# Performance work log

Hardware: AMD Instinct MI355X
Metric: run time of the kernel (lower is better)

The kernel has to match this reference:

```python
import jax, jax.numpy as jnp
import numpy as np

H = 5  # LSTM hidden size


def _lstm_layer(x, Wih, Whh, bih, bhh):
    # x: [B, T, D]; Wih: [4H, D]; Whh: [4H, H]; biases: [4H]
    B, T, _ = x.shape
    # precompute input contribution with one big GEMM (torch gate order i,f,g,o)
    xg = jnp.einsum('btd,gd->btg', x, Wih) + bih + bhh  # [B,T,4H]
    xg = jnp.swapaxes(xg, 0, 1)  # [T,B,4H]
    WhhT = Whh.T

    def step(carry, g_t):
        h, c = carry
        g = g_t + h @ WhhT
        i, f, gg, o = jnp.split(g, 4, axis=-1)
        i = jax.nn.sigmoid(i)
        f = jax.nn.sigmoid(f)
        gg = jnp.tanh(gg)
        o = jax.nn.sigmoid(o)
        c = f * c + i * gg
        h = o * jnp.tanh(c)
        return (h, c), h

    h0 = jnp.zeros((B, H), x.dtype)
    c0 = jnp.zeros((B, H), x.dtype)
    _, hs = jax.lax.scan(step, (h0, c0), xg)
    return jnp.swapaxes(hs, 0, 1)  # [B,T,H]


def _stacked_lstm(x, params):
    for (Wih, Whh, bih, bhh) in params:
        x = _lstm_layer(x, Wih, Whh, bih, bhh)
    return x


def setup_inputs() -> dict:
    key = jax.random.key(0)
    ks = jax.random.split(key, 24)
    B, T, D = 512, 1024, 225
    s = 1.0 / np.sqrt(H)

    def u(k, shape):
        return jax.random.uniform(k, shape, jnp.float32, -s, s)

    inp = {"x": jax.random.normal(ks[0], (B, T, D), jnp.float32)}
    # lstm1: layer0 input D=225, layer1 input H=5
    inp["l1_Wih0"] = u(ks[1], (4 * H, D)); inp["l1_Whh0"] = u(ks[2], (4 * H, H))
    inp["l1_bih0"] = u(ks[3], (4 * H,)); inp["l1_bhh0"] = u(ks[4], (4 * H,))
    inp["l1_Wih1"] = u(ks[5], (4 * H, H)); inp["l1_Whh1"] = u(ks[6], (4 * H, H))
    inp["l1_bih1"] = u(ks[7], (4 * H,)); inp["l1_bhh1"] = u(ks[8], (4 * H,))
    inp["fc1_W"] = u(ks[9], (H, H)); inp["fc1_b"] = u(ks[10], (H,))
    # lstm2: both layers input H=5
    inp["l2_Wih0"] = u(ks[11], (4 * H, H)); inp["l2_Whh0"] = u(ks[12], (4 * H, H))
    inp["l2_bih0"] = u(ks[13], (4 * H,)); inp["l2_bhh0"] = u(ks[14], (4 * H,))
    inp["l2_Wih1"] = u(ks[15], (4 * H, H)); inp["l2_Whh1"] = u(ks[16], (4 * H, H))
    inp["l2_bih1"] = u(ks[17], (4 * H,)); inp["l2_bhh1"] = u(ks[18], (4 * H,))
    inp["fc2_W"] = u(ks[19], (H, H)); inp["fc2_b"] = u(ks[20], (H,))
    return inp


def reference(x, l1_Wih0, l1_Whh0, l1_bih0, l1_bhh0,
              l1_Wih1, l1_Whh1, l1_bih1, l1_bhh1,
              fc1_W, fc1_b,
              l2_Wih0, l2_Whh0, l2_bih0, l2_bhh0,
              l2_Wih1, l2_Whh1, l2_bih1, l2_bhh1,
              fc2_W, fc2_b):
    # dropout layers are identity in inference mode
    h = _stacked_lstm(x, [(l1_Wih0, l1_Whh0, l1_bih0, l1_bhh0),
                          (l1_Wih1, l1_Whh1, l1_bih1, l1_bhh1)])
    h = jax.nn.relu(h @ fc1_W.T + fc1_b)
    h = _stacked_lstm(h, [(l2_Wih0, l2_Whh0, l2_bih0, l2_bhh0),
                          (l2_Wih1, l2_Whh1, l2_bih1, l2_bhh1)])
    return jax.nn.sigmoid(h @ fc2_W.T + fc2_b)
```

## Files before the change

### kernel.cpp

```cpp
#include <hip/hip_runtime.h>
#include <math.h>

#define T_STEPS 1024
#define B_SIZE  512
#define D_IN    225
#define WT_K    228
#define LOG2E   1.4426950408889634f

typedef float f32x2 __attribute__((ext_vector_type(2)));

__device__ __forceinline__ float fexp2(float x) {
#if __has_builtin(__builtin_amdgcn_exp2f)
  return __builtin_amdgcn_exp2f(x);
#else
  return exp2f(x);
#endif
}
__device__ __forceinline__ float frcp(float x) {
#if __has_builtin(__builtin_amdgcn_rcpf)
  return __builtin_amdgcn_rcpf(x);
#else
  return 1.0f / x;
#endif
}
#define SIG(x) frcp(1.0f + fexp2((x) * (-LOG2E)))
#define TH(x)  fmaf(2.0f, frcp(1.0f + fexp2((x) * (-2.0f * LOG2E))), -1.0f)

#define GL16(gp, lp) __builtin_amdgcn_global_load_lds(                          \
    (const __attribute__((address_space(1))) void*)(gp),                        \
    (__attribute__((address_space(3))) void*)(lp), 16, 0, 0)
#define GL4(gp, lp)  __builtin_amdgcn_global_load_lds(                          \
    (const __attribute__((address_space(1))) void*)(gp),                        \
    (__attribute__((address_space(3))) void*)(lp), 4, 0, 0)

#define WAIT_VM0() do {                                                         \
    asm volatile("s_waitcnt vmcnt(0)" ::: "memory");                            \
    __builtin_amdgcn_sched_barrier(0);                                          \
  } while (0)
#define WAIT_VM10() do {                                                        \
    asm volatile("s_waitcnt vmcnt(10)" ::: "memory");                           \
    __builtin_amdgcn_sched_barrier(0);                                          \
  } while (0)

__global__ __launch_bounds__(256)
void prep_wt(const float* __restrict__ Wih, const float* __restrict__ bih,
             const float* __restrict__ bhh, float* __restrict__ wt2)
{
  int i = blockIdx.x * 256 + threadIdx.x;
  int g = i / WT_K, kk = i - g * WT_K;
  float v = 0.f;
  if (g < 20 && kk < 225) v = Wih[g * 225 + kk];
  if (i >= 4560 && i < 4580) v = bih[i - 4560] + bhh[i - 4560];
  wt2[i] = v;
}

__global__ __launch_bounds__(256)
void xg_gemm(const float* __restrict__ x, const float* __restrict__ wtg,
             float* __restrict__ xg)
{
  __shared__ __align__(16) float xs[64 * 228];
  __shared__ __align__(16) float wt[4608];
  __shared__ float xs224[64];
  const int tid  = threadIdx.x;
  const int lane = tid & 63;
  const int w    = __builtin_amdgcn_readfirstlane(tid >> 6);

  for (int m = w; m < 18; m += 4)
    GL16(wtg + m * 256 + lane * 4, wt + m * 256);

  {
    const uint32_t base = (uint32_t)blockIdx.x * 57600u;
    const uint32_t lim  = 471859184u;
    for (int m = w; m < 57; m += 4) {
      uint32_t c   = (uint32_t)(m * 64 + lane);
      uint32_t r   = __umulhi(c, 75350304u);
      uint32_t off = (c << 4) - 12u * r;
      uint32_t ga  = base + off;
      ga = (ga < lim) ? ga : lim;
      GL16((const char*)x + ga, (char*)xs + m * 1024);
    }
    if (w == 0)
      GL4(x + (size_t)blockIdx.x * 14400 + lane * 225 + 224, xs224 + lane);
  }
  __syncthreads();

  const float* wr = wt + (5 * w) * WT_K;
  float acc[5];
#pragma unroll
  for (int j = 0; j < 5; ++j) acc[j] = wt[4560 + 5 * w + j];
  const float* xr = xs + lane * 228;

#pragma unroll 8
  for (int kb = 0; kb < 224; kb += 4) {
    const float4 xv = *(const float4*)(xr + kb);
#pragma unroll
    for (int j = 0; j < 5; ++j) {
      const float4 wv = *(const float4*)(wr + j * WT_K + kb);
      acc[j] = fmaf(xv.x, wv.x, acc[j]);
      acc[j] = fmaf(xv.y, wv.y, acc[j]);
      acc[j] = fmaf(xv.z, wv.z, acc[j]);
      acc[j] = fmaf(xv.w, wv.w, acc[j]);
    }
  }
  {
    float xl = xs224[lane];
#pragma unroll
    for (int j = 0; j < 5; ++j) acc[j] = fmaf(xl, wr[j * WT_K + 224], acc[j]);
  }
  float* op = xg + ((size_t)blockIdx.x * 64 + lane) * 20 + w;
#pragma unroll
  for (int j = 0; j < 5; ++j) op[4 * j] = acc[j];
}

__global__ __launch_bounds__(64)
void lstm_fused(const float* __restrict__ xg, float* __restrict__ out,
              const float* __restrict__ l1_Whh0,
              const float* __restrict__ l1_Wih1, const float* __restrict__ l1_Whh1,
              const float* __restrict__ l1_bih1, const float* __restrict__ l1_bhh1,
              const float* __restrict__ fc1_W,  const float* __restrict__ fc1_b,
              const float* __restrict__ l2_Wih0, const float* __restrict__ l2_Whh0,
              const float* __restrict__ l2_bih0, const float* __restrict__ l2_bhh0,
              const float* __restrict__ l2_Wih1, const float* __restrict__ l2_Whh1,
              const float* __restrict__ l2_bih1, const float* __restrict__ l2_bhh1,
              const float* __restrict__ fc2_W,  const float* __restrict__ fc2_b)
{
  __shared__ __align__(16) float xq[2][2][1280];
  __shared__ float outb[2][64][5];
  const int lane  = threadIdx.x & 63;
  const int half  = lane >> 5;
  const int l32   = lane & 31;
  const int stage = (l32 < 30) ? (l32 / 5) : 6;
  const int u     = (l32 < 30) ? (l32 - stage * 5) : 0;
  const int b0    = blockIdx.x * 2;

  const bool is_l0   = (stage == 0);
  const bool is_relu = (stage == 2);
  const bool is_fc   = (stage == 2) || (stage == 5);
  const bool is_fc2  = (stage == 5);

  float wi[4][5] = {}, wh[4][5] = {}, bs[4] = {};
  if (stage == 0) {
#pragma unroll
    for (int q = 0; q < 4; ++q)
#pragma unroll
      for (int j = 0; j < 5; ++j) wh[q][j] = l1_Whh0[(u + 5 * q) * 5 + j];
  } else if (stage == 1) {
#pragma unroll
    for (int q = 0; q < 4; ++q) {
#pragma unroll
      for (int j = 0; j < 5; ++j) {
        wi[q][j] = l1_Wih1[(u + 5 * q) * 5 + j];
        wh[q][j] = l1_Whh1[(u + 5 * q) * 5 + j];
      }
      bs[q] = l1_bih1[u + 5 * q] + l1_bhh1[u + 5 * q];
    }
  } else if (stage == 3) {
#pragma unroll
    for (int q = 0; q < 4; ++q) {
#pragma unroll
      for (int j = 0; j < 5; ++j) {
        wi[q][j] = l2_Wih0[(u + 5 * q) * 5 + j];
        wh[q][j] = l2_Whh0[(u + 5 * q) * 5 + j];
      }
      bs[q] = l2_bih0[u + 5 * q] + l2_bhh0[u + 5 * q];
    }
  } else if (stage == 4) {
#pragma unroll
    for (int q = 0; q < 4; ++q) {
#pragma unroll
      for (int j = 0; j < 5; ++j) {
        wi[q][j] = l2_Wih1[(u + 5 * q) * 5 + j];
        wh[q][j] = l2_Whh1[(u + 5 * q) * 5 + j];
      }
      bs[q] = l2_bih1[u + 5 * q] + l2_bhh1[u + 5 * q];
    }
  } else if (stage == 2) {
#pragma unroll
    for (int j = 0; j < 5; ++j) wi[0][j] = fc1_W[u * 5 + j];
    bs[0] = fc1_b[u];
  } else if (stage == 5) {
#pragma unroll
    for (int j = 0; j < 5; ++j) wi[0][j] = fc2_W[u * 5 + j];
    bs[0] = fc2_b[u];
  }

  f32x2 wi01[5], wi23[5], wh01[5], wh23[5];
#pragma unroll
  for (int j = 0; j < 5; ++j) {
    wi01[j] = f32x2{wi[0][j], wi[1][j]};
    wi23[j] = f32x2{wi[2][j], wi[3][j]};
    wh01[j] = f32x2{wh[0][j], wh[1][j]};
    wh23[j] = f32x2{wh[2][j], wh[3][j]};
  }
  const f32x2 bs01 = f32x2{bs[0], bs[1]};
  const f32x2 bs23 = f32x2{bs[2], bs[3]};

  int ii[5], ih[5];
  const int bse = half * 32;
  const int inb = (stage >= 1 && stage <= 5) ? (stage - 1) * 5 : 0;
  const int hb_ = (stage <= 5) ? stage * 5 : 0;
#pragma unroll
  for (int j = 0; j < 5; ++j) {
    ii[j] = (bse + inb + j) * 4;
    ih[j] = (bse + hb_ + j) * 4;
  }

  const float* obf = &outb[0][0][0];
  float* outbase = out + (size_t)b0 * T_STEPS * 5;
  int lof[10], ofs[10];
  bool fg1[10], fg2[10];
#pragma unroll
  for (int i2 = 0; i2 < 10; ++i2) {
    int idx = i2 * 64 + lane;
    int e  = (idx >= 320) ? 1 : 0;
    int r  = idx - e * 320;
    int tq = r / 5;
    int j2 = r - tq * 5;
    lof[i2] = e * 320 + (((tq - 5) & 63) * 5) + j2;
    ofs[i2] = e * (T_STEPS * 5) + tq * 5 + j2;
    fg1[i2] = (tq >= 5);
    fg2[i2] = (tq < 5);
  }

  const float* src0 = xg + (size_t)(b0 + 0) * T_STEPS * 20;
  const float* src1 = xg + (size_t)(b0 + 1) * T_STEPS * 20;

#define STAGE_CHUNK(CH, BUF)                                                   \
  { const float* s0_ = src0 + (CH) * 1280;                                     \
    const float* s1_ = src1 + (CH) * 1280;                                     \
    float* d0_ = &xq[BUF][0][0];                                               \
    float* d1_ = &xq[BUF][1][0];                                               \
    _Pragma("unroll")                                                          \
    for (int m = 0; m < 5; ++m) {                                              \
      GL16(s0_ + m * 256 + lane * 4, d0_ + m * 256);                           \
      GL16(s1_ + m * 256 + lane * 4, d1_ + m * 256);                           \
    } }

#define TICK(QV, GUARDED, KVAL)                                                \
  { const int hvi_ = __float_as_int(hv);                                       \
    float inx[5], hhx[5];                                                      \
    _Pragma("unroll")                                                          \
    for (int j = 0; j < 5; ++j) {                                              \
      inx[j] = __int_as_float(__builtin_amdgcn_ds_bpermute(ii[j], hvi_));      \
      hhx[j] = __int_as_float(__builtin_amdgcn_ds_bpermute(ih[j], hvi_));      \
    }                                                                          \
    f32x2 a01 = is_l0 ? f32x2{(QV).x, (QV).y} : bs01;                          \
    f32x2 a23 = is_l0 ? f32x2{(QV).z, (QV).w} : bs23;                          \
    f32x2 b01, b23;                                                            \
    { const f32x2 h0 = f32x2{hhx[0], hhx[0]};                                  \
      b01 = wh01[0] * h0; b23 = wh23[0] * h0; }                                \
    _Pragma("unroll")                                                          \
    for (int j = 0; j < 5; ++j) {                                              \
      const f32x2 xj = f32x2{inx[j], inx[j]};                                  \
      a01 = __builtin_elementwise_fma(wi01[j], xj, a01);                       \
      a23 = __builtin_elementwise_fma(wi23[j], xj, a23);                       \
    }                                                                          \
    _Pragma("unroll")                                                          \
    for (int j = 1; j < 5; ++j) {                                              \
      const f32x2 hj = f32x2{hhx[j], hhx[j]};                                  \
      b01 = __builtin_elementwise_fma(wh01[j], hj, b01);                       \
      b23 = __builtin_elementwise_fma(wh23[j], hj, b23);                       \
    }                                                                          \
    const f32x2 pre01 = a01 + b01, pre23 = a23 + b23;                          \
    float i_ = SIG(pre01.x), f_ = SIG(pre01.y);                                \
    float g_ = TH(pre23.x),  o_ = SIG(pre23.y);                                \
    float cn = fmaf(f_, c, i_ * g_);                                           \
    float hl = o_ * TH(cn);                                                    \
    float fx = is_relu ? fmaxf(pre01.x, 0.0f) : i_;                            \
    float hn = is_fc ? fx : hl;                                                \
    if (GUARDED) { bool ok = (KVAL) >= stage; c = ok ? cn : c; hv = ok ? hn : hv; } \
    else         { c = cn; hv = hn; }                                          \
    if (is_fc2) outb[half][((KVAL) + 59) & 63][u] = i_;                        \
  }

#define LQ(T) (*(const float4*)(xqb + 20 * (T)))
#define MINQ(X) (((X) > 63) ? 63 : (X))

#define CHUNK_BODY(GUARDED)                                                    \
  { float4 qA = LQ(0), qB = LQ(1), qC = LQ(2), qD = LQ(3);                     \
    _Pragma("unroll")                                                          \
    for (int g4 = 0; g4 < 16; ++g4) {                                          \
      const int kk = g4 * 4;                                                   \
      TICK(qA, GUARDED, kk + 0)                                                \
      qA = LQ(MINQ(kk + 4));                                                   \
      TICK(qB, GUARDED, kk + 1)                                                \
      qB = LQ(MINQ(kk + 5));                                                   \
      TICK(qC, GUARDED, kk + 2)                                                \
      qC = LQ(MINQ(kk + 6));                                                   \
      TICK(qD, GUARDED, kk + 3)                                                \
      qD = LQ(MINQ(kk + 7));                                                   \
    } }

#define FLUSH(TBASE, MODE)                                                     \
  { _Pragma("unroll")                                                          \
    for (int i2 = 0; i2 < 10; ++i2) {                                          \
      float v = obf[lof[i2]];                                                  \
      bool ok = (MODE == 0) || ((MODE == 1) ? fg1[i2] : fg2[i2]);              \
      if (ok) outbase[ofs[i2] + (TBASE) * 5] = v;                              \
    } }

  float hv = 0.f, c = 0.f;

  STAGE_CHUNK(0, 0)
  WAIT_VM0();

  {
    STAGE_CHUNK(1, 1)
    const float* xqb = &xq[0][half][4 * u];
    CHUNK_BODY(true)
    FLUSH(-5, 1)
    WAIT_VM10();
  }
  for (int ch = 1; ch < 16; ++ch) {
    if (ch < 15) STAGE_CHUNK(ch + 1, (ch + 1) & 1)
    const float* xqb = &xq[ch & 1][half][4 * u];
    CHUNK_BODY(false)
    FLUSH(ch * 64 - 5, 0)
    WAIT_VM10();
  }
  {
    const float* xqb = &xq[0][half][4 * u];
    float4 qZ = LQ(0);
    TICK(qZ, false, 0)
    TICK(qZ, false, 1)
    TICK(qZ, false, 2)
    TICK(qZ, false, 3)
    TICK(qZ, false, 4)
    FLUSH(T_STEPS - 5, 2)
  }

#undef STAGE_CHUNK
#undef TICK
#undef LQ
#undef MINQ
#undef CHUNK_BODY
#undef FLUSH
}

extern "C" void kernel_launch(void* const* d_in, const int* in_sizes, int n_in,
                              void* d_out, int out_size, void* d_ws, size_t ws_size,
                              hipStream_t stream)
{
  const float* x        = (const float*)d_in[0];
  const float* l1_Wih0  = (const float*)d_in[1];
  const float* l1_Whh0  = (const float*)d_in[2];
  const float* l1_bih0  = (const float*)d_in[3];
  const float* l1_bhh0  = (const float*)d_in[4];
  const float* l1_Wih1  = (const float*)d_in[5];
  const float* l1_Whh1  = (const float*)d_in[6];
  const float* l1_bih1  = (const float*)d_in[7];
  const float* l1_bhh1  = (const float*)d_in[8];
  const float* fc1_W    = (const float*)d_in[9];
  const float* fc1_b    = (const float*)d_in[10];
  const float* l2_Wih0  = (const float*)d_in[11];
  const float* l2_Whh0  = (const float*)d_in[12];
  const float* l2_bih0  = (const float*)d_in[13];
  const float* l2_bhh0  = (const float*)d_in[14];
  const float* l2_Wih1  = (const float*)d_in[15];
  const float* l2_Whh1  = (const float*)d_in[16];
  const float* l2_bih1  = (const float*)d_in[17];
  const float* l2_bhh1  = (const float*)d_in[18];
  const float* fc2_W    = (const float*)d_in[19];
  const float* fc2_b    = (const float*)d_in[20];

  float* xg   = (float*)d_ws;
  float* wtws = xg + 10485760;
  float* out  = (float*)d_out;

  prep_wt<<<dim3(18), dim3(256), 0, stream>>>(l1_Wih0, l1_bih0, l1_bhh0, wtws);

  xg_gemm<<<dim3((B_SIZE * T_STEPS) / 64), dim3(256), 0, stream>>>(x, wtws, xg);

  lstm_fused<<<dim3(B_SIZE / 2), dim3(64), 0, stream>>>(
      xg, out, l1_Whh0, l1_Wih1, l1_Whh1, l1_bih1, l1_bhh1,
      fc1_W, fc1_b, l2_Wih0, l2_Whh0, l2_bih0, l2_bhh0,
      l2_Wih1, l2_Whh1, l2_bih1, l2_bhh1, fc2_W, fc2_b);
}
```

Measured before the change: 414.9 us.

## Interleave two independent batch recurrences per wavefront and halve the grid

After: 649.2 us. 56.5% more time.

```diff
diff --git a/kernel.cpp b/kernel.cpp
--- a/kernel.cpp
+++ b/kernel.cpp
@@ -37,8 +37,8 @@
     asm volatile("s_waitcnt vmcnt(0)" ::: "memory");                            \
     __builtin_amdgcn_sched_barrier(0);                                          \
   } while (0)
-#define WAIT_VM10() do {                                                        \
-    asm volatile("s_waitcnt vmcnt(10)" ::: "memory");                           \
+#define WAIT_VM20() do {                                                        \
+    asm volatile("s_waitcnt vmcnt(20)" ::: "memory");                           \
     __builtin_amdgcn_sched_barrier(0);                                          \
   } while (0)
 
@@ -124,14 +124,14 @@
               const float* __restrict__ l2_bih1, const float* __restrict__ l2_bhh1,
               const float* __restrict__ fc2_W,  const float* __restrict__ fc2_b)
 {
-  __shared__ __align__(16) float xq[2][2][1280];
-  __shared__ float outb[2][64][5];
+  __shared__ __align__(16) float xq[2][4][1280];
+  __shared__ float outb[4][64][5];
   const int lane  = threadIdx.x & 63;
   const int half  = lane >> 5;
   const int l32   = lane & 31;
   const int stage = (l32 < 30) ? (l32 / 5) : 6;
   const int u     = (l32 < 30) ? (l32 - stage * 5) : 0;
-  const int b0    = blockIdx.x * 2;
+  const int b0    = blockIdx.x * 4;
 
   const bool is_l0   = (stage == 0);
   const bool is_relu = (stage == 2);
@@ -207,133 +207,131 @@
 
   const float* obf = &outb[0][0][0];
   float* outbase = out + (size_t)b0 * T_STEPS * 5;
-  int lof[10], ofs[10];
-  bool fg1[10], fg2[10];
-#pragma unroll
-  for (int i2 = 0; i2 < 10; ++i2) {
+  int lof[20], ofsv[20];
+  bool fgA[20], fgB[20];
+#pragma unroll
+  for (int i2 = 0; i2 < 20; ++i2) {
     int idx = i2 * 64 + lane;
-    int e  = (idx >= 320) ? 1 : 0;
-    int r  = idx - e * 320;
+    int m  = idx / 320;
+    int r  = idx - m * 320;
     int tq = r / 5;
     int j2 = r - tq * 5;
-    lof[i2] = e * 320 + (((tq - 5) & 63) * 5) + j2;
-    ofs[i2] = e * (T_STEPS * 5) + tq * 5 + j2;
-    fg1[i2] = (tq >= 5);
-    fg2[i2] = (tq < 5);
-  }
-
-  const float* src0 = xg + (size_t)(b0 + 0) * T_STEPS * 20;
-  const float* src1 = xg + (size_t)(b0 + 1) * T_STEPS * 20;
+    lof[i2]  = m * 320 + (((tq - 5) & 63) * 5) + j2;
+    ofsv[i2] = m * (T_STEPS * 5) + tq * 5 + j2;
+    fgA[i2]  = (tq >= 5);
+    fgB[i2]  = (tq < 5);
+  }
+
+  const float* srcp0 = xg + (size_t)(b0 + 0) * T_STEPS * 20;
+  const float* srcp1 = xg + (size_t)(b0 + 1) * T_STEPS * 20;
+  const float* srcp2 = xg + (size_t)(b0 + 2) * T_STEPS * 20;
+  const float* srcp3 = xg + (size_t)(b0 + 3) * T_STEPS * 20;
 
 #define STAGE_CHUNK(CH, BUF)                                                   \
-  { const float* s0_ = src0 + (CH) * 1280;                                     \
-    const float* s1_ = src1 + (CH) * 1280;                                     \
-    float* d0_ = &xq[BUF][0][0];                                               \
-    float* d1_ = &xq[BUF][1][0];                                               \
-    _Pragma("unroll")                                                          \
+  { _Pragma("unroll")                                                          \
     for (int m = 0; m < 5; ++m) {                                              \
-      GL16(s0_ + m * 256 + lane * 4, d0_ + m * 256);                           \
-      GL16(s1_ + m * 256 + lane * 4, d1_ + m * 256);                           \
+      GL16(srcp0 + (CH) * 1280 + m * 256 + lane * 4, &xq[BUF][0][m * 256]);    \
+      GL16(srcp1 + (CH) * 1280 + m * 256 + lane * 4, &xq[BUF][1][m * 256]);    \
+      GL16(srcp2 + (CH) * 1280 + m * 256 + lane * 4, &xq[BUF][2][m * 256]);    \
+      GL16(srcp3 + (CH) * 1280 + m * 256 + lane * 4, &xq[BUF][3][m * 256]);    \
     } }
 
-#define TICK(QV, GUARDED, KVAL)                                                \
-  { const int hvi_ = __float_as_int(hv);                                       \
-    float inx[5], hhx[5];                                                      \
+#define TICKP(Q, IN, HH, HV, CC, OB, XQB, GUARDED, KVAL)                       \
+  { f32x2 a01 = is_l0 ? f32x2{(Q).x, (Q).y} : bs01;                            \
+    f32x2 a23 = is_l0 ? f32x2{(Q).z, (Q).w} : bs23;                            \
     _Pragma("unroll")                                                          \
     for (int j = 0; j < 5; ++j) {                                              \
-      inx[j] = __int_as_float(__builtin_amdgcn_ds_bpermute(ii[j], hvi_));      \
-      hhx[j] = __int_as_float(__builtin_amdgcn_ds_bpermute(ih[j], hvi_));      \
-    }                                                                          \
-    f32x2 a01 = is_l0 ? f32x2{(QV).x, (QV).y} : bs01;                          \
-    f32x2 a23 = is_l0 ? f32x2{(QV).z, (QV).w} : bs23;                          \
-    f32x2 b01, b23;                                                            \
-    { const f32x2 h0 = f32x2{hhx[0], hhx[0]};                                  \
-      b01 = wh01[0] * h0; b23 = wh23[0] * h0; }                                \
-    _Pragma("unroll")                                                          \
-    for (int j = 0; j < 5; ++j) {                                              \
-      const f32x2 xj = f32x2{inx[j], inx[j]};                                  \
+      const f32x2 xj = f32x2{IN[j], IN[j]};                                    \
       a01 = __builtin_elementwise_fma(wi01[j], xj, a01);                       \
       a23 = __builtin_elementwise_fma(wi23[j], xj, a23);                       \
     }                                                                          \
+    f32x2 b01, b23;                                                            \
+    { const f32x2 h0 = f32x2{HH[0], HH[0]};                                    \
+      b01 = wh01[0] * h0; b23 = wh23[0] * h0; }                                \
     _Pragma("unroll")                                                          \
     for (int j = 1; j < 5; ++j) {                                              \
-      const f32x2 hj = f32x2{hhx[j], hhx[j]};                                  \
+      const f32x2 hj = f32x2{HH[j], HH[j]};                                    \
       b01 = __builtin_elementwise_fma(wh01[j], hj, b01);                       \
       b23 = __builtin_elementwise_fma(wh23[j], hj, b23);                       \
     }                                                                          \
     const f32x2 pre01 = a01 + b01, pre23 = a23 + b23;                          \
     float i_ = SIG(pre01.x), f_ = SIG(pre01.y);                                \
     float g_ = TH(pre23.x),  o_ = SIG(pre23.y);                                \
-    float cn = fmaf(f_, c, i_ * g_);                                           \
+    float cn = fmaf(f_, CC, i_ * g_);                                          \
     float hl = o_ * TH(cn);                                                    \
     float fx = is_relu ? fmaxf(pre01.x, 0.0f) : i_;                            \
     float hn = is_fc ? fx : hl;                                                \
-    if (GUARDED) { bool ok = (KVAL) >= stage; c = ok ? cn : c; hv = ok ? hn : hv; } \
-    else         { c = cn; hv = hn; }                                          \
-    if (is_fc2) outb[half][((KVAL) + 59) & 63][u] = i_;                        \
-  }
-
-#define LQ(T) (*(const float4*)(xqb + 20 * (T)))
-#define MINQ(X) (((X) > 63) ? 63 : (X))
-
-#define CHUNK_BODY(GUARDED)                                                    \
-  { float4 qA = LQ(0), qB = LQ(1), qC = LQ(2), qD = LQ(3);                     \
-    _Pragma("unroll")                                                          \
-    for (int g4 = 0; g4 < 16; ++g4) {                                          \
-      const int kk = g4 * 4;                                                   \
-      TICK(qA, GUARDED, kk + 0)                                                \
-      qA = LQ(MINQ(kk + 4));                                                   \
-      TICK(qB, GUARDED, kk + 1)                                                \
-      qB = LQ(MINQ(kk + 5));                                                   \
-      TICK(qC, GUARDED, kk + 2)                                                \
-      qC = LQ(MINQ(kk + 6));                                                   \
-      TICK(qD, GUARDED, kk + 3)                                                \
-      qD = LQ(MINQ(kk + 7));                                                   \
-    } }
+    if (GUARDED) { bool ok = (KVAL) >= stage; CC = ok ? cn : CC; HV = ok ? hn : HV; } \
+    else         { CC = cn; HV = hn; }                                         \
+    if (is_fc2) OB[(((KVAL) + 59) & 63) * 5 + u] = i_;                         \
+    { const int hvi_ = __float_as_int(HV);                                     \
+      _Pragma("unroll")                                                        \
+      for (int j = 0; j < 5; ++j) {                                            \
+        IN[j] = __int_as_float(__builtin_amdgcn_ds_bpermute(ii[j], hvi_));     \
+        HH[j] = __int_as_float(__builtin_amdgcn_ds_bpermute(ih[j], hvi_));     \
+      } }                                                                      \
+    { int nq_ = (KVAL) + 1; nq_ = (nq_ > 63) ? 63 : nq_;                       \
+      Q = *(const float4*)((XQB) + 20 * nq_); }                                \
+  }
 
 #define FLUSH(TBASE, MODE)                                                     \
   { _Pragma("unroll")                                                          \
-    for (int i2 = 0; i2 < 10; ++i2) {                                          \
+    for (int i2 = 0; i2 < 20; ++i2) {                                          \
       float v = obf[lof[i2]];                                                  \
-      bool ok = (MODE == 0) || ((MODE == 1) ? fg1[i2] : fg2[i2]);              \
-      if (ok) outbase[ofs[i2] + (TBASE) * 5] = v;                              \
+      bool ok = (MODE == 0) || ((MODE == 1) ? fgA[i2] : fgB[i2]);              \
+      if (ok) outbase[ofsv[i2] + (TBASE) * 5] = v;                             \
     } }
 
-  float hv = 0.f, c = 0.f;
+  float hvA = 0.f, cA = 0.f, hvB = 0.f, cB = 0.f;
+  float inA[5] = {0,0,0,0,0}, hhA[5] = {0,0,0,0,0};
+  float inB[5] = {0,0,0,0,0}, hhB[5] = {0,0,0,0,0};
+  float4 qA, qB;
+  float* obA = &outb[half][0][0];
+  float* obB = &outb[2 + half][0][0];
 
   STAGE_CHUNK(0, 0)
   WAIT_VM0();
 
   {
     STAGE_CHUNK(1, 1)
-    const float* xqb = &xq[0][half][4 * u];
-    CHUNK_BODY(true)
+    const float* xqA = &xq[0][half][4 * u];
+    const float* xqB = &xq[0][2 + half][4 * u];
+    qA = *(const float4*)xqA;
+    qB = *(const float4*)xqB;
+#pragma unroll 2
+    for (int kk = 0; kk < 64; ++kk) {
+      TICKP(qA, inA, hhA, hvA, cA, obA, xqA, true, kk)
+      TICKP(qB, inB, hhB, hvB, cB, obB, xqB, true, kk)
+    }
     FLUSH(-5, 1)
-    WAIT_VM10();
+    WAIT_VM20();
   }
   for (int ch = 1; ch < 16; ++ch) {
     if (ch < 15) STAGE_CHUNK(ch + 1, (ch + 1) & 1)
-    const float* xqb = &xq[ch & 1][half][4 * u];
-    CHUNK_BODY(false)
+    const float* xqA = &xq[ch & 1][half][4 * u];
+    const float* xqB = &xq[ch & 1][2 + half][4 * u];
+    qA = *(const float4*)xqA;
+    qB = *(const float4*)xqB;
+#pragma unroll 2
+    for (int kk = 0; kk < 64; ++kk) {
+      TICKP(qA, inA, hhA, hvA, cA, obA, xqA, false, kk)
+      TICKP(qB, inB, hhB, hvB, cB, obB, xqB, false, kk)
+    }
     FLUSH(ch * 64 - 5, 0)
-    WAIT_VM10();
+    WAIT_VM20();
   }
   {
-    const float* xqb = &xq[0][half][4 * u];
-    float4 qZ = LQ(0);
-    TICK(qZ, false, 0)
-    TICK(qZ, false, 1)
-    TICK(qZ, false, 2)
-    TICK(qZ, false, 3)
-    TICK(qZ, false, 4)
+    const float* xqA = &xq[0][half][4 * u];
+    const float* xqB = &xq[0][2 + half][4 * u];
+    for (int kk = 0; kk < 5; ++kk) {
+      TICKP(qA, inA, hhA, hvA, cA, obA, xqA, false, kk)
+      TICKP(qB, inB, hhB, hvB, cB, obB, xqB, false, kk)
+    }
     FLUSH(T_STEPS - 5, 2)
   }
 
 #undef STAGE_CHUNK
-#undef TICK
-#undef LQ
-#undef MINQ
-#undef CHUNK_BODY
+#undef TICKP
 #undef FLUSH
 }
 
@@ -371,7 +369,7 @@
 
   xg_gemm<<<dim3((B_SIZE * T_STEPS) / 64), dim3(256), 0, stream>>>(x, wtws, xg);
 
-  lstm_fused<<<dim3(B_SIZE / 2), dim3(64), 0, stream>>>(
+  lstm_fused<<<dim3(B_SIZE / 4), dim3(64), 0, stream>>>(
       xg, out, l1_Whh0, l1_Wih1, l1_Whh1, l1_bih1, l1_bhh1,
       fc1_W, fc1_b, l2_Wih0, l2_Whh0, l2_bih0, l2_bhh0,
       l2_Wih1, l2_Whh1, l2_bih1, l2_bhh1, fc2_W, fc2_b);
```
